# Kernel tuning notes

Measured on AMD Instinct MI355X. Metric: run time of the kernel, lower is better.

The kernel has to match this reference:

```python
import jax, jax.numpy as jnp
import numpy as np

ROPE_DIM = 16      # RotaryEmbedding(dim=16)
MAX_FREQ = 256.0   # freqs_for='pixel'
NUM_HEADS = 16


def _axis_freqs(n):
    # pixel mode: base freqs = linspace(1, max_freq/2, dim//2) * pi, pos = linspace(-1, 1, n)
    base = jnp.linspace(1.0, MAX_FREQ / 2.0, ROPE_DIM // 2) * jnp.pi  # (8,)
    pos = jnp.linspace(-1.0, 1.0, n)                                   # (n,)
    f = pos[:, None] * base[None, :]                                   # (n, 8)
    return jnp.repeat(f, 2, axis=-1)                                   # (n, 16) interleaved pairs


def axial_freqs(T, H, W):
    ft = jnp.broadcast_to(_axis_freqs(T)[:, None, None, :], (T, H, W, ROPE_DIM))
    fh = jnp.broadcast_to(_axis_freqs(H)[None, :, None, :], (T, H, W, ROPE_DIM))
    fw = jnp.broadcast_to(_axis_freqs(W)[None, None, :, :], (T, H, W, ROPE_DIM))
    return jnp.concatenate([ft, fh, fw], axis=-1)  # (T, H, W, 48)


def rotate_half(x):
    # interleaved pairs: (..., d*2) -> rotate each (x1, x2) -> (-x2, x1)
    x = x.reshape(*x.shape[:-1], -1, 2)
    x1, x2 = x[..., 0], x[..., 1]
    return jnp.stack([-x2, x1], axis=-1).reshape(*x.shape[:-2], -1)


def apply_rope(freqs, t):
    # freqs: (T, H, W, rot_dim); t: (B, nh, T, H, W, hd); rotate first rot_dim dims
    rd = freqs.shape[-1]
    tm, tr = t[..., :rd], t[..., rd:]
    tm = tm * jnp.cos(freqs) + rotate_half(tm) * jnp.sin(freqs)
    return jnp.concatenate([tm, tr], axis=-1)


def setup_inputs() -> dict:
    key = jax.random.key(0)
    k1, k2, k3, k4 = jax.random.split(key, 4)
    B, N, C = 2, 2048, 1152
    return {
        "x": jax.random.normal(k1, (B, N, C), dtype=jnp.float32),
        "Wqkv": jax.random.normal(k2, (C, 3 * C), dtype=jnp.float32) * 0.02,
        "Wproj": jax.random.normal(k3, (C, C), dtype=jnp.float32) * 0.02,
        "bproj": jax.random.normal(k4, (C,), dtype=jnp.float32) * 0.02,
        "T": 8, "H": 16, "W": 16,
    }


def reference(x, Wqkv, Wproj, bproj, T, H, W):
    B, N, C = x.shape
    nh = NUM_HEADS
    hd = C // nh
    qkv = (x @ Wqkv).reshape(B, N, 3, nh, hd).transpose(2, 0, 3, 1, 4)  # (3, B, nh, N, hd)
    q, k, v = qkv[0], qkv[1], qkv[2]
    # tokens -> video grid
    q = q.reshape(B, nh, T, H, W, hd)
    k = k.reshape(B, nh, T, H, W, hd)
    freqs = axial_freqs(T, H, W)  # (T, H, W, 48)
    q = apply_rope(freqs, q).reshape(B, nh, N, hd)
    k = apply_rope(freqs, k).reshape(B, nh, N, hd)
    # SDPA (no mask, no dropout in eval / kv_cache=None path)
    scale = 1.0 / np.sqrt(hd)
    attn = jax.nn.softmax(jnp.einsum('bhqd,bhkd->bhqk', q, k) * scale, axis=-1)
    o = jnp.einsum('bhqk,bhkd->bhqd', attn, v)  # (B, nh, N, hd)
    o = o.transpose(0, 2, 1, 3).reshape(B, N, C)
    return o @ Wproj + bproj
```

## Files before the change

### kernel.cpp

```cpp
#include <hip/hip_runtime.h>
#include <hip/hip_bf16.h>

#define B_   2
#define N_   2048
#define C_   1152
#define NH   16
#define HD   72
#define HDP  96
#define HDV  80
#define QSTR 3584
#define KROW 104
#define VROW 72
#define KVB  64

typedef __attribute__((ext_vector_type(8))) short bf16x8;
typedef __attribute__((ext_vector_type(4))) float f32x4;

__device__ __forceinline__ short f2bf(float f) {
  union { float fv; unsigned int u; } v; v.fv = f;
  unsigned int r = v.u + 0x7fffu + ((v.u >> 16) & 1u);
  return (short)(r >> 16);
}

__device__ __forceinline__ float bf2f(short s) {
  union { unsigned u; float f; } v; v.u = ((unsigned)(unsigned short)s) << 16;
  return v.f;
}

__device__ __forceinline__ unsigned pack_bf16(float a, float b) {
  union { __hip_bfloat162 h; unsigned u; } c;
  c.h = __float22bfloat162_rn(make_float2(a, b));
  return c.u;
}

__device__ __forceinline__ void gload_lds16(const short* g, short* l) {
  __builtin_amdgcn_global_load_lds(
      (const __attribute__((address_space(1))) unsigned int*)g,
      (__attribute__((address_space(3))) unsigned int*)l, 16, 0, 0);
}

__global__ void cvt_bf16(const float* __restrict__ in, short* __restrict__ out, int n4) {
  int i = blockIdx.x * 256 + threadIdx.x;
  if (i < n4) {
    float4 v = ((const float4*)in)[i];
    short4 s;
    s.x = f2bf(v.x); s.y = f2bf(v.y); s.z = f2bf(v.z); s.w = f2bf(v.w);
    ((short4*)out)[i] = s;
  }
}

__global__ void transpose_cvt(const float* __restrict__ src, short* __restrict__ dst,
                              int R, int Cc, int Np) {
  __shared__ float tile[32][33];
  const int c0 = blockIdx.x * 32, r0 = blockIdx.y * 32;
  const int tx = threadIdx.x, ty = threadIdx.y;
  for (int i = ty; i < 32; i += 8)
    tile[i][tx] = (c0 + tx < Cc) ? src[(long)(r0 + i) * Cc + c0 + tx] : 0.f;
  __syncthreads();
  for (int i = ty; i < 32; i += 8)
    dst[(long)(c0 + i) * R + r0 + tx] = f2bf(tile[tx][i]);
}

template<bool BIAS, bool OBF>
__global__ __launch_bounds__(256, 2) void gemm_bt(
    const short* __restrict__ A, const short* __restrict__ Bt,
    void* __restrict__ Cv, const float* __restrict__ bias,
    int M, int N, int K) {
  __shared__ __align__(16) short As[2][128 * 32];
  __shared__ __align__(16) short Bs[2][128 * 32];
  const int t = threadIdx.x;
  const int lane = t & 63, wid = t >> 6;
  const int fr = lane & 15, fq = lane >> 4;

  int lin = blockIdx.y * gridDim.x + blockIdx.x;
  const int q8 = (int)(gridDim.x * gridDim.y) >> 3;
  lin = (lin & 7) * q8 + (lin >> 3);
  const int bm = lin / (int)gridDim.x;
  const int bn = lin - bm * (int)gridDim.x;

  const int wr = (wid >> 1) * 64, wc = (wid & 1) * 64;

  const int srow = t >> 2;
  const int scol = (t & 3) * 8;
  const short* Ag = A + (long)(bm * 128 + srow) * K + scol;
  const short* Bg = Bt + (long)(bn * 128 + srow) * K + scol;

  f32x4 acc[4][4] = {};

  auto STAGE = [&](int kt, int bufi) {
    gload_lds16(Ag + kt * 32,                &As[bufi][t * 8]);
    gload_lds16(Ag + kt * 32 + (long)64 * K, &As[bufi][2048 + t * 8]);
    gload_lds16(Bg + kt * 32,                &Bs[bufi][t * 8]);
    gload_lds16(Bg + kt * 32 + (long)64 * K, &Bs[bufi][2048 + t * 8]);
  };

  const int NKT = K / 32;
  STAGE(0, 0);

  for (int kt = 0; kt < NKT; ++kt) {
    const int cur = kt & 1;
    if (kt + 1 < NKT) {
      STAGE(kt + 1, cur ^ 1);
      asm volatile("s_waitcnt vmcnt(4)" ::: "memory");
    } else {
      asm volatile("s_waitcnt vmcnt(0)" ::: "memory");
    }
    __builtin_amdgcn_s_barrier();

    bf16x8 af[4], bf[4];
    #pragma unroll
    for (int i = 0; i < 4; ++i)
      af[i] = *(const bf16x8*)(&As[cur][(wr + i * 16 + fr) * 32 + fq * 8]);
    #pragma unroll
    for (int j = 0; j < 4; ++j)
      bf[j] = *(const bf16x8*)(&Bs[cur][(wc + j * 16 + fr) * 32 + fq * 8]);
    __builtin_amdgcn_s_setprio(1);
    #pragma unroll
    for (int i = 0; i < 4; ++i)
      #pragma unroll
      for (int j = 0; j < 4; ++j)
        acc[i][j] = __builtin_amdgcn_mfma_f32_16x16x32_bf16(af[i], bf[j], acc[i][j], 0, 0, 0);
    __builtin_amdgcn_s_setprio(0);
    __builtin_amdgcn_s_barrier();
  }

  #pragma unroll
  for (int i = 0; i < 4; ++i) {
    #pragma unroll
    for (int j = 0; j < 4; ++j) {
      const long row0 = (long)bm * 128 + wr + i * 16 + fq * 4;
      const int col = bn * 128 + wc + j * 16 + fr;
      const float bv = BIAS ? bias[col] : 0.f;
      #pragma unroll
      for (int r = 0; r < 4; ++r) {
        const float val = acc[i][j][r] + bv;
        if constexpr (OBF)
          ((short*)Cv)[(row0 + r) * (long)N + col] = f2bf(val);
        else
          ((float*)Cv)[(row0 + r) * (long)N + col] = val;
      }
    }
  }
}

__global__ __launch_bounds__(512, 2) void gemm_bt256(
    const short* __restrict__ A, const short* __restrict__ Bt,
    short* __restrict__ Cv, int M, int N, int K) {
  __shared__ __align__(16) short As[2][256 * 64];
  __shared__ __align__(16) short Bs[2][256 * 64];
  const int t = threadIdx.x;
  const int lane = t & 63, wid = t >> 6;
  const int fr = lane & 15, fq = lane >> 4;
  const int wm = wid >> 2, wn = wid & 3;
  const int rx = fr & 7;

  int lin = blockIdx.y * gridDim.x + blockIdx.x;
  const int q8 = (int)(gridDim.x * gridDim.y) >> 3;
  lin = (lin & 7) * q8 + (lin >> 3);
  const int bm = lin / (int)gridDim.x;
  const int bn = lin - bm * (int)gridDim.x;

  int soff[4];
  #pragma unroll
  for (int r = 0; r < 4; ++r) {
    const int p = r * 512 + t;
    const int row = p >> 3, pc = p & 7;
    soff[r] = row * K + (pc ^ (row & 7)) * 8;
  }
  const short* Ag = A + (long)bm * 256 * K;
  const short* Bg = Bt + (long)bn * 256 * K;

  f32x4 acc[8][4] = {};

  const int NKT = K / 64;
  #pragma unroll
  for (int r = 0; r < 4; ++r)
    gload_lds16(Ag + soff[r], &As[0][(r * 512 + t) * 8]);
  #pragma unroll
  for (int r = 0; r < 4; ++r)
    gload_lds16(Bg + soff[r], &Bs[0][(r * 512 + t) * 8]);

  for (int kt = 0; kt < NKT; ++kt) {
    const int cur = kt & 1;
    const bool pre = (kt + 1 < NKT);
    asm volatile("s_waitcnt vmcnt(0)" ::: "memory");
    __builtin_amdgcn_s_barrier();
    const short* Ac = &As[cur][0];
    const short* Bc = &Bs[cur][0];
    bf16x8 af[4][2], bf0[2][2], bf1[2][2];

    if (pre) {
      #pragma unroll
      for (int r = 0; r < 4; ++r)
        gload_lds16(Ag + soff[r] + (kt + 1) * 64, &As[cur ^ 1][(r * 512 + t) * 8]);
    }
    #pragma unroll
    for (int i = 0; i < 4; ++i)
      #pragma unroll
      for (int kk = 0; kk < 2; ++kk)
        af[i][kk] = *(const bf16x8*)(Ac + (wm * 128 + i * 16 + fr) * 64 + (((kk * 4 + fq) ^ rx) * 8));
    #pragma unroll
    for (int j = 0; j < 2; ++j)
      #pragma unroll
      for (int kk = 0; kk < 2; ++kk)
        bf0[j][kk] = *(const bf16x8*)(Bc + (wn * 64 + j * 16 + fr) * 64 + (((kk * 4 + fq) ^ rx) * 8));
    __builtin_amdgcn_s_setprio(1);
    #pragma unroll
    for (int i = 0; i < 4; ++i)
      #pragma unroll
      for (int j = 0; j < 2; ++j)
        #pragma unroll
        for (int kk = 0; kk < 2; ++kk)
          acc[i][j] = __builtin_amdgcn_mfma_f32_16x16x32_bf16(af[i][kk], bf0[j][kk], acc[i][j], 0, 0, 0);
    __builtin_amdgcn_s_setprio(0);

    if (pre) {
      #pragma unroll
      for (int r = 0; r < 4; ++r)
        gload_lds16(Bg + soff[r] + (kt + 1) * 64, &Bs[cur ^ 1][(r * 512 + t) * 8]);
    }
    #pragma unroll
    for (int j = 0; j < 2; ++j)
      #pragma unroll
      for (int kk = 0; kk < 2; ++kk)
        bf1[j][kk] = *(const bf16x8*)(Bc + (wn * 64 + 32 + j * 16 + fr) * 64 + (((kk * 4 + fq) ^ rx) * 8));
    __builtin_amdgcn_s_setprio(1);
    #pragma unroll
    for (int i = 0; i < 4; ++i)
      #pragma unroll
      for (int j = 0; j < 2; ++j)
        #pragma unroll
        for (int kk = 0; kk < 2; ++kk)
          acc[i][2 + j] = __builtin_amdgcn_mfma_f32_16x16x32_bf16(af[i][kk], bf1[j][kk], acc[i][2 + j], 0, 0, 0);
    __builtin_amdgcn_s_setprio(0);

    #pragma unroll
    for (int i = 0; i < 4; ++i)
      #pragma unroll
      for (int kk = 0; kk < 2; ++kk)
        af[i][kk] = *(const bf16x8*)(Ac + (wm * 128 + 64 + i * 16 + fr) * 64 + (((kk * 4 + fq) ^ rx) * 8));
    __builtin_amdgcn_s_setprio(1);
    #pragma unroll
    for (int i = 0; i < 4; ++i)
      #pragma unroll
      for (int j = 0; j < 2; ++j)
        #pragma unroll
        for (int kk = 0; kk < 2; ++kk)
          acc[4 + i][j] = __builtin_amdgcn_mfma_f32_16x16x32_bf16(af[i][kk], bf0[j][kk], acc[4 + i][j], 0, 0, 0);
    __builtin_amdgcn_s_setprio(0);

    __builtin_amdgcn_s_setprio(1);
    #pragma unroll
    for (int i = 0; i < 4; ++i)
      #pragma unroll
      for (int j = 0; j < 2; ++j)
        #pragma unroll
        for (int kk = 0; kk < 2; ++kk)
          acc[4 + i][2 + j] = __builtin_amdgcn_mfma_f32_16x16x32_bf16(af[i][kk], bf1[j][kk], acc[4 + i][2 + j], 0, 0, 0);
    __builtin_amdgcn_s_setprio(0);
  }

  #pragma unroll
  for (int mi = 0; mi < 8; ++mi) {
    #pragma unroll
    for (int j = 0; j < 4; ++j) {
      const long row0 = (long)bm * 256 + wm * 128 + (mi >> 2) * 64 + (mi & 3) * 16 + fq * 4;
      const int col = bn * 256 + wn * 64 + j * 16 + fr;
      #pragma unroll
      for (int r = 0; r < 4; ++r)
        Cv[(row0 + r) * (long)N + col] = f2bf(acc[mi][j][r]);
    }
  }
}

__global__ __launch_bounds__(256) void rope_pack(
    const short* __restrict__ QKV, short* __restrict__ Qp,
    short* __restrict__ Kp, short* __restrict__ Vt) {
  const int blk = blockIdx.x;
  const int nt = blk & 15;
  const int h = (blk >> 4) & 15;
  const int b = blk >> 8;
  const int t = threadIdx.x;
  const int n0 = nt * 128;
  const float qscale = 0.17002324f;
  const float PI = 3.14159265358979323846f;

  for (int which = 0; which < 2; ++which) {
    short* dst = which ? Kp : Qp;
    const float sc = which ? 1.0f : qscale;
    for (int idx = t; idx < 128 * 48; idx += 256) {
      const int r = idx / 48;
      const int p = idx - r * 48;
      const int n = n0 + r;
      float vx = 0.f, vy = 0.f;
      if (p < 36) {
        short2 v2 = *(const short2*)(QKV + ((long)(b * N_ + n)) * QSTR + which * C_ + h * HD + 2 * p);
        vx = bf2f(v2.x); vy = bf2f(v2.y);
      }
      float o0 = vx, o1 = vy;
      if (p < 24) {
        float pos;
        if (p < 8)       pos = -1.f + (2.f / 7.f)  * (float)(n >> 8);
        else if (p < 16) pos = -1.f + (2.f / 15.f) * (float)((n >> 4) & 15);
        else             pos = -1.f + (2.f / 15.f) * (float)(n & 15);
        const float base = (1.f + (127.f / 7.f) * (float)(p & 7)) * PI;
        const float f = pos * base;
        const float cs = cosf(f), sn = sinf(f);
        o0 = vx * cs - vy * sn;
        o1 = vy * cs + vx * sn;
      }
      short2 ov; ov.x = f2bf(o0 * sc); ov.y = f2bf(o1 * sc);
      *(short2*)(dst + (((long)(b * NH + h)) * N_ + n) * HDP + 2 * p) = ov;
    }
  }

  __shared__ short vt[128][82];
  for (int idx = t; idx < 128 * 40; idx += 256) {
    const int r = idx / 40, p = idx - r * 40;
    short2 v2; v2.x = 0; v2.y = 0;
    if (p < 36)
      v2 = *(const short2*)(QKV + ((long)(b * N_ + n0 + r)) * QSTR + 2 * C_ + h * HD + 2 * p);
    *(short2*)(&vt[r][2 * p]) = v2;
  }
  __syncthreads();
  for (int idx = t; idx < HDV * 128; idx += 256) {
    const int d = idx >> 7, nn = idx & 127;
    const int c = nn & 31;
    const int nsrc = (nn & 96) | (((c >> 2) & 1) * 16 + ((c >> 3) & 3) * 4 + (c & 3));
    Vt[(((long)(b * NH + h)) * HDV + d) * N_ + n0 + nn] = vt[nsrc][d];
  }
}

__global__ __launch_bounds__(256, 3) void attn(
    const short* __restrict__ Qp, const short* __restrict__ Kp,
    const short* __restrict__ Vt, short* __restrict__ Aproj) {
  __shared__ __align__(16) short Ks[2][KVB * KROW];
  __shared__ __align__(16) short Vs[2][HDV * VROW];
  int blk = blockIdx.x;
  blk = (blk & 7) * 64 + (blk >> 3);
  const int qt = blk & 15;
  const int h = (blk >> 4) & 15;
  const int b = blk >> 8;
  const int t = threadIdx.x, lane = t & 63, wid = t >> 6;
  const int fr = lane & 15, fq = lane >> 4;

  const long bh = (long)(b * NH + h);
  const short* Qg = Qp + (bh * N_ + qt * 128) * HDP;
  const short* Kg = Kp + bh * N_ * HDP;
  const short* Vg = Vt + bh * HDV * N_;

  int koff[4];
  #pragma unroll
  for (int it = 0; it < 4; ++it) {
    const int p = it * 256 + t;
    const int row = p / 13, c = p - row * 13;
    koff[it] = row * HDP + (c < 12 ? c * 8 : 0);
  }
  int voff[3];
  #pragma unroll
  for (int it = 0; it < 3; ++it) {
    const int p = it * 256 + t;
    const int row = p / 9, c = p - row * 9;
    voff[it] = row * N_ + (c < 8 ? c * 8 : 0);
  }

  bf16x8 qf[2][3];
  #pragma unroll
  for (int i = 0; i < 2; ++i)
    #pragma unroll
    for (int kk = 0; kk < 3; ++kk)
      qf[i][kk] = *(const bf16x8*)(Qg + (wid * 32 + i * 16 + fr) * HDP + kk * 32 + fq * 8);

  f32x4 accO[2][5] = {};
  float l_[2] = {0.f, 0.f};

  auto STAGE = [&](int kt, int bufi) {
    const short* Ksrc = Kg + (long)kt * KVB * HDP;
    const short* Vsrc = Vg + kt * KVB;
    short* KD = &Ks[bufi][0];
    short* VD = &Vs[bufi][0];
    #pragma unroll
    for (int it = 0; it < 4; ++it)
      if (it < 3 || t < 64)
        gload_lds16(Ksrc + koff[it], KD + (it * 256 + t) * 8);
    #pragma unroll
    for (int it = 0; it < 3; ++it)
      if (it < 2 || t < 208)
        gload_lds16(Vsrc + voff[it], VD + (it * 256 + t) * 8);
  };

  STAGE(0, 0);
  asm volatile("s_waitcnt vmcnt(0)" ::: "memory");
  __syncthreads();

  for (int kt = 0; kt < 32; ++kt) {
    const int cur = kt & 1;
    if (kt < 31) STAGE(kt + 1, cur ^ 1);
    const short* KsC = &Ks[cur][0];
    const short* VsC = &Vs[cur][0];

    f32x4 s[2][4] = {};
    __builtin_amdgcn_s_setprio(1);
    #pragma unroll
    for (int j = 0; j < 4; ++j) {
      #pragma unroll
      for (int kk = 0; kk < 3; ++kk) {
        bf16x8 kf = *(const bf16x8*)(KsC + (j * 16 + fr) * KROW + (kk * 4 + fq) * 8);
        s[0][j] = __builtin_amdgcn_mfma_f32_16x16x32_bf16(kf, qf[0][kk], s[0][j], 0, 0, 0);
        s[1][j] = __builtin_amdgcn_mfma_f32_16x16x32_bf16(kf, qf[1][kk], s[1][j], 0, 0, 0);
      }
    }
    __builtin_amdgcn_s_setprio(0);

    #pragma unroll
    for (int i = 0; i < 2; ++i) {
      float psum = 0.f;
      #pragma unroll
      for (int j = 0; j < 4; ++j)
        #pragma unroll
        for (int r = 0; r < 4; ++r) {
          const float p = __builtin_amdgcn_exp2f(s[i][j][r]);
          s[i][j][r] = p;
          psum += p;
        }
      l_[i] += psum;
    }

    __builtin_amdgcn_s_setprio(1);
    #pragma unroll
    for (int g = 0; g < 2; ++g) {
      union { unsigned u[4]; bf16x8 v; } pf0, pf1;
      pf0.u[0] = pack_bf16(s[0][2 * g][0],     s[0][2 * g][1]);
      pf0.u[1] = pack_bf16(s[0][2 * g][2],     s[0][2 * g][3]);
      pf0.u[2] = pack_bf16(s[0][2 * g + 1][0], s[0][2 * g + 1][1]);
      pf0.u[3] = pack_bf16(s[0][2 * g + 1][2], s[0][2 * g + 1][3]);
      pf1.u[0] = pack_bf16(s[1][2 * g][0],     s[1][2 * g][1]);
      pf1.u[1] = pack_bf16(s[1][2 * g][2],     s[1][2 * g][3]);
      pf1.u[2] = pack_bf16(s[1][2 * g + 1][0], s[1][2 * g + 1][1]);
      pf1.u[3] = pack_bf16(s[1][2 * g + 1][2], s[1][2 * g + 1][3]);
      #pragma unroll
      for (int jd = 0; jd < 5; ++jd) {
        bf16x8 vf = *(const bf16x8*)(VsC + (jd * 16 + fr) * VROW + (g * 4 + fq) * 8);
        accO[0][jd] = __builtin_amdgcn_mfma_f32_16x16x32_bf16(pf0.v, vf, accO[0][jd], 0, 0, 0);
        accO[1][jd] = __builtin_amdgcn_mfma_f32_16x16x32_bf16(pf1.v, vf, accO[1][jd], 0, 0, 0);
      }
    }
    __builtin_amdgcn_s_setprio(0);
    asm volatile("s_waitcnt vmcnt(0)" ::: "memory");
    __syncthreads();
  }

  #pragma unroll
  for (int i = 0; i < 2; ++i) {
    l_[i] += __shfl_xor(l_[i], 16);
    l_[i] += __shfl_xor(l_[i], 32);
  }
  float linv[2] = {1.f / l_[0], 1.f / l_[1]};
  #pragma unroll
  for (int i = 0; i < 2; ++i) {
    float li[4];
    #pragma unroll
    for (int r = 0; r < 4; ++r) li[r] = __shfl(linv[i], fq * 4 + r);
    #pragma unroll
    for (int r = 0; r < 4; ++r) {
      const long n = qt * 128 + wid * 32 + i * 16 + fq * 4 + r;
      #pragma unroll
      for (int jd = 0; jd < 5; ++jd) {
        const int d = jd * 16 + fr;
        if (d < HD)
          Aproj[((long)b * N_ + n) * C_ + h * HD + d] = f2bf(accO[i][jd][r] * li[r]);
      }
    }
  }
}

extern "C" void kernel_launch(void* const* d_in, const int* in_sizes, int n_in,
                              void* d_out, int out_size, void* d_ws, size_t ws_size,
                              hipStream_t stream) {
  const float* x     = (const float*)d_in[0];
  const float* Wqkv  = (const float*)d_in[1];
  const float* Wproj = (const float*)d_in[2];
  const float* bproj = (const float*)d_in[3];
  float* out = (float*)d_out;

  char* ws = (char*)d_ws;
  short* QKVb = (short*)ws;         size_t off = (size_t)4096 * QSTR * 2;
  short* xb  = (short*)(ws + off);  off += (size_t)4096 * 1152 * 2;
  short* Wt  = (short*)(ws + off);  off += (size_t)QSTR * 1152 * 2;
  short* Wpt = (short*)(ws + off);  off += (size_t)1152 * 1152 * 2;
  short* Qp  = (short*)(ws + off);  off += (size_t)B_ * NH * N_ * HDP * 2;
  short* Kp  = (short*)(ws + off);  off += (size_t)B_ * NH * N_ * HDP * 2;
  short* Vt  = (short*)(ws + off);  off += (size_t)B_ * NH * HDV * N_ * 2;
  short* Ap  = (short*)(ws + off);  off += (size_t)4096 * 1152 * 2;

  cvt_bf16<<<(4096 * 1152 / 4 + 255) / 256, 256, 0, stream>>>(x, xb, 4096 * 1152 / 4);
  transpose_cvt<<<dim3(QSTR / 32, 1152 / 32), dim3(32, 8), 0, stream>>>(Wqkv, Wt, 1152, 3456, QSTR);
  transpose_cvt<<<dim3(1152 / 32, 1152 / 32), dim3(32, 8), 0, stream>>>(Wproj, Wpt, 1152, 1152, 1152);
  gemm_bt256<<<dim3(QSTR / 256, 4096 / 256), 512, 0, stream>>>(
      xb, Wt, QKVb, 4096, QSTR, 1152);
  rope_pack<<<B_ * NH * (N_ / 128), 256, 0, stream>>>(QKVb, Qp, Kp, Vt);
  attn<<<B_ * NH * (N_ / 128), 256, 0, stream>>>(Qp, Kp, Vt, Ap);
  gemm_bt<true, false><<<dim3(1152 / 128, 4096 / 128), 256, 0, stream>>>(
      Ap, Wpt, (void*)out, bproj, 4096, 1152, 1152);
}
```

Before: 187.1 us.

## Triple-buffer attention K/V staging and fuse prep conversion kernels

```diff
diff --git a/kernel.cpp b/kernel.cpp
--- a/kernel.cpp
+++ b/kernel.cpp
@@ -12,6 +12,10 @@
 #define KROW 104
 #define VROW 72
 #define KVB  64
+#define KCH  832
+#define VCH  720
+#define TCH  1552
+#define WCH  388
 
 typedef __attribute__((ext_vector_type(8))) short bf16x8;
 typedef __attribute__((ext_vector_type(4))) float f32x4;
@@ -39,26 +43,35 @@
       (__attribute__((address_space(3))) unsigned int*)l, 16, 0, 0);
 }
 
-__global__ void cvt_bf16(const float* __restrict__ in, short* __restrict__ out, int n4) {
-  int i = blockIdx.x * 256 + threadIdx.x;
-  if (i < n4) {
-    float4 v = ((const float4*)in)[i];
+__global__ __launch_bounds__(256) void prep(
+    const float* __restrict__ x, short* __restrict__ xb,
+    const float* __restrict__ Wqkv, short* __restrict__ Wt,
+    const float* __restrict__ Wproj, short* __restrict__ Wpt) {
+  int bid = blockIdx.x;
+  if (bid < 4608) {
+    const int i = bid * 256 + threadIdx.x;
+    float4 v = ((const float4*)x)[i];
     short4 s;
     s.x = f2bf(v.x); s.y = f2bf(v.y); s.z = f2bf(v.z); s.w = f2bf(v.w);
-    ((short4*)out)[i] = s;
-  }
-}
-
-__global__ void transpose_cvt(const float* __restrict__ src, short* __restrict__ dst,
-                              int R, int Cc, int Np) {
+    ((short4*)xb)[i] = s;
+    return;
+  }
+  bid -= 4608;
+  const float* src; short* dst; int Cc, bx, by;
+  if (bid < 4032) {
+    bx = bid % 112; by = bid / 112; src = Wqkv; dst = Wt; Cc = 3456;
+  } else {
+    bid -= 4032;
+    bx = bid % 36; by = bid / 36; src = Wproj; dst = Wpt; Cc = 1152;
+  }
   __shared__ float tile[32][33];
-  const int c0 = blockIdx.x * 32, r0 = blockIdx.y * 32;
-  const int tx = threadIdx.x, ty = threadIdx.y;
+  const int c0 = bx * 32, r0 = by * 32;
+  const int tx = threadIdx.x & 31, ty = threadIdx.x >> 5;
   for (int i = ty; i < 32; i += 8)
     tile[i][tx] = (c0 + tx < Cc) ? src[(long)(r0 + i) * Cc + c0 + tx] : 0.f;
   __syncthreads();
   for (int i = ty; i < 32; i += 8)
-    dst[(long)(c0 + i) * R + r0 + tx] = f2bf(tile[tx][i]);
+    dst[(long)(c0 + i) * 1152 + r0 + tx] = f2bf(tile[tx][i]);
 }
 
 template<bool BIAS, bool OBF>
@@ -331,11 +344,10 @@
   }
 }
 
-__global__ __launch_bounds__(256, 3) void attn(
+__global__ __launch_bounds__(256, 2) void attn(
     const short* __restrict__ Qp, const short* __restrict__ Kp,
     const short* __restrict__ Vt, short* __restrict__ Aproj) {
-  __shared__ __align__(16) short Ks[2][KVB * KROW];
-  __shared__ __align__(16) short Vs[2][HDV * VROW];
+  __shared__ __align__(16) short KV[3][TCH * 8];
   int blk = blockIdx.x;
   blk = (blk & 7) * 64 + (blk >> 3);
   const int qt = blk & 15;
@@ -349,19 +361,22 @@
   const short* Kg = Kp + bh * N_ * HDP;
   const short* Vg = Vt + bh * HDV * N_;
 
-  int koff[4];
-  #pragma unroll
-  for (int it = 0; it < 4; ++it) {
-    const int p = it * 256 + t;
-    const int row = p / 13, c = p - row * 13;
-    koff[it] = row * HDP + (c < 12 ? c * 8 : 0);
-  }
-  int voff[3];
-  #pragma unroll
-  for (int it = 0; it < 3; ++it) {
-    const int p = it * 256 + t;
-    const int row = p / 9, c = p - row * 9;
-    voff[it] = row * N_ + (c < 8 ? c * 8 : 0);
+  const short* sb[7];
+  int sstr[7];
+  #pragma unroll
+  for (int it = 0; it < 7; ++it) {
+    int g = wid * WCH + (it < 6 ? it * 64 + lane : 384 + lane);
+    if (g >= TCH) g = TCH - 1;
+    if (g < KCH) {
+      const int r = g / 13, c = g - r * 13;
+      sb[it] = Kg + r * HDP + (c < 12 ? c * 8 : 0);
+      sstr[it] = KVB * HDP;
+    } else {
+      const int v = g - KCH;
+      const int r = v / 9, c = v - r * 9;
+      sb[it] = Vg + r * N_ + (c < 8 ? c * 8 : 0);
+      sstr[it] = KVB;
+    }
   }
 
   bf16x8 qf[2][3];
@@ -375,29 +390,25 @@
   float l_[2] = {0.f, 0.f};
 
   auto STAGE = [&](int kt, int bufi) {
-    const short* Ksrc = Kg + (long)kt * KVB * HDP;
-    const short* Vsrc = Vg + kt * KVB;
-    short* KD = &Ks[bufi][0];
-    short* VD = &Vs[bufi][0];
-    #pragma unroll
-    for (int it = 0; it < 4; ++it)
-      if (it < 3 || t < 64)
-        gload_lds16(Ksrc + koff[it], KD + (it * 256 + t) * 8);
-    #pragma unroll
-    for (int it = 0; it < 3; ++it)
-      if (it < 2 || t < 208)
-        gload_lds16(Vsrc + voff[it], VD + (it * 256 + t) * 8);
+    short* D = &KV[bufi][0];
+    #pragma unroll
+    for (int it = 0; it < 6; ++it)
+      gload_lds16(sb[it] + kt * sstr[it], D + (wid * WCH + it * 64 + lane) * 8);
+    if (lane < 4)
+      gload_lds16(sb[6] + kt * sstr[6], D + (wid * WCH + 384 + lane) * 8);
   };
 
   STAGE(0, 0);
-  asm volatile("s_waitcnt vmcnt(0)" ::: "memory");
-  __syncthreads();
+  STAGE(1, 1);
 
   for (int kt = 0; kt < 32; ++kt) {
-    const int cur = kt & 1;
-    if (kt < 31) STAGE(kt + 1, cur ^ 1);
-    const short* KsC = &Ks[cur][0];
-    const short* VsC = &Vs[cur][0];
+    if (kt < 31) asm volatile("s_waitcnt vmcnt(7)" ::: "memory");
+    else         asm volatile("s_waitcnt vmcnt(0)" ::: "memory");
+    __builtin_amdgcn_s_barrier();
+    if (kt < 30) STAGE(kt + 2, (kt + 2) % 3);
+
+    const short* KsC = &KV[kt % 3][0];
+    const short* VsC = KsC + KCH * 8;
 
     f32x4 s[2][4] = {};
     __builtin_amdgcn_s_setprio(1);
@@ -446,8 +457,6 @@
       }
     }
     __builtin_amdgcn_s_setprio(0);
-    asm volatile("s_waitcnt vmcnt(0)" ::: "memory");
-    __syncthreads();
   }
 
   #pragma unroll
@@ -493,9 +502,7 @@
   short* Vt  = (short*)(ws + off);  off += (size_t)B_ * NH * HDV * N_ * 2;
   short* Ap  = (short*)(ws + off);  off += (size_t)4096 * 1152 * 2;
 
-  cvt_bf16<<<(4096 * 1152 / 4 + 255) / 256, 256, 0, stream>>>(x, xb, 4096 * 1152 / 4);
-  transpose_cvt<<<dim3(QSTR / 32, 1152 / 32), dim3(32, 8), 0, stream>>>(Wqkv, Wt, 1152, 3456, QSTR);
-  transpose_cvt<<<dim3(1152 / 32, 1152 / 32), dim3(32, 8), 0, stream>>>(Wproj, Wpt, 1152, 1152, 1152);
+  prep<<<4608 + 4032 + 1296, 256, 0, stream>>>(x, xb, Wqkv, Wt, Wproj, Wpt);
   gemm_bt256<<<dim3(QSTR / 256, 4096 / 256), 512, 0, stream>>>(
       xb, Wt, QKVb, 4096, QSTR, 1152);
   rope_pack<<<B_ * NH * (N_ / 128), 256, 0, stream>>>(QKVb, Qp, Kp, Vt);
```

Result: faster. 179.1 us (-4.2%).
